# Kernel optimization log

Hardware: AMD Instinct MI355X
Metric: run time of the kernel (lower is better)

## Reference

```python
import jax, jax.numpy as jnp
import numpy as np

B, T, D = 4, 2048, 512
H, P = 8, 16
DH = D // H
C = 512
HF = WF = 64
RADIUS = 0.08


def setup_inputs() -> dict:
    key = jax.random.key(0)
    ks = jax.random.split(key, 8)
    s = 0.02
    return {
        "q": jax.random.normal(ks[0], (B, T, D), jnp.float32),
        "fmap": jax.random.normal(ks[1], (B, C, HF, WF), jnp.float32),
        "ref_xy": jax.random.uniform(ks[2], (B, T, 2), jnp.float32),
        # params ((in,out) layout; equals torch Linear with W.T)
        "Wv": jax.random.normal(ks[3], (C, D), jnp.float32) * s,      # 1x1 conv, no bias
        "W_off": jax.random.normal(ks[4], (D, H * P * 2), jnp.float32) * s,
        "b_off": jnp.zeros((H * P * 2,), jnp.float32),
        "W_w": jax.random.normal(ks[5], (D, H * P), jnp.float32) * s,
        "b_w": jnp.zeros((H * P,), jnp.float32),
        "W_out": jax.random.normal(ks[6], (D, D), jnp.float32) * s,
        "b_out": jnp.zeros((D,), jnp.float32),
    }


def _deform_attn(q, fmap, ref_xy, Wv, W_off, b_off, W_w, b_w, W_out, b_out):
    Bq, Tq, Dm = q.shape
    _, Cc, Hf, Wf = fmap.shape
    dh = Dm // H
    # value projection (1x1 conv) then split heads: (B,H,dh,Hf,Wf)
    v = jnp.einsum("bchw,cd->bdhw", fmap, Wv).reshape(Bq, H, dh, Hf, Wf)
    # flatten spatial for gather: (B,H,Hf*Wf,dh)
    vflat = v.transpose(0, 1, 3, 4, 2).reshape(Bq, H, Hf * Wf, dh)

    off = (q @ W_off + b_off).reshape(Bq, Tq, H, P, 2)
    attn = jax.nn.softmax((q @ W_w + b_w).reshape(Bq, Tq, H, P), axis=-1)

    samp = ref_xy[:, :, None, None, :] + RADIUS * off   # (B,T,H,P,2) in ~[0,1]
    g = samp * 2.0 - 1.0                                 # grid coords in [-1,1]
    # align_corners=True mapping to pixel coords
    ix = (g[..., 0] + 1.0) * 0.5 * (Wf - 1)              # (B,T,H,P)
    iy = (g[..., 1] + 1.0) * 0.5 * (Hf - 1)
    ix0 = jnp.floor(ix)
    iy0 = jnp.floor(iy)
    fx = ix - ix0
    fy = iy - iy0
    ix0i = ix0.astype(jnp.int32)
    iy0i = iy0.astype(jnp.int32)

    def corner(xi, yi, wgt):
        # wgt: bilinear weight * attention weight, (B,T,H,P)
        valid = (xi >= 0) & (xi < Wf) & (yi >= 0) & (yi < Hf)  # zeros padding
        xi_c = jnp.clip(xi, 0, Wf - 1)
        yi_c = jnp.clip(yi, 0, Hf - 1)
        idx = (yi_c * Wf + xi_c).transpose(0, 2, 1, 3).reshape(Bq, H, Tq * P)
        gat = jnp.take_along_axis(vflat, idx[..., None], axis=2)  # (B,H,T*P,dh)
        wm = (wgt * valid).transpose(0, 2, 1, 3).reshape(Bq, H, Tq * P)
        return gat * wm[..., None]

    # fold softmax weights into bilinear corner weights, then sum over points
    feat = (
        corner(ix0i,     iy0i,     (1 - fx) * (1 - fy) * attn)
        + corner(ix0i + 1, iy0i,     fx * (1 - fy) * attn)
        + corner(ix0i,     iy0i + 1, (1 - fx) * fy * attn)
        + corner(ix0i + 1, iy0i + 1, fx * fy * attn)
    )  # (B,H,T*P,dh)
    ctx = feat.reshape(Bq, H, Tq, P, dh).sum(axis=3)     # (B,H,T,dh)
    ctx = ctx.transpose(0, 2, 1, 3).reshape(Bq, Tq, Dm)  # concat heads
    return ctx @ W_out + b_out


def reference(q, fmap, ref_xy, Wv, W_off, b_off, W_w, b_w, W_out, b_out):
    return _deform_attn(q, fmap, ref_xy, Wv, W_off, b_off, W_w, b_w, W_out, b_out)
```

## Files before the change

kernel.cpp:

```cpp
#include <hip/hip_runtime.h>
#include <hip/hip_bf16.h>
#include <math.h>

constexpr int Bsz = 4, T = 2048, Hh = 8;
constexpr int HFi = 64, WFi = 64;
constexpr float RADIUS = 0.08f;

typedef __bf16 bf16x8 __attribute__((ext_vector_type(8)));
typedef float f32x4 __attribute__((ext_vector_type(4)));
typedef unsigned short u16x8 __attribute__((ext_vector_type(8)));

typedef const __attribute__((address_space(1))) void* gcptr;
typedef __attribute__((address_space(3))) void* lptr;

#define GLOAD_LDS16(g, l) \
  __builtin_amdgcn_global_load_lds((gcptr)(const void*)(g), (lptr)(void*)(l), 16, 0, 0)

union BU { __hip_bfloat16 b; unsigned short u; };

__global__ __launch_bounds__(256) void prep_kernel(
    const float* __restrict__ q, __hip_bfloat16* __restrict__ qsplit,
    const float* __restrict__ W_off, const float* __restrict__ W_w,
    const float* __restrict__ b_off, const float* __restrict__ b_w,
    __hip_bfloat16* __restrict__ Wcat, float* __restrict__ bias_cat,
    const float* __restrict__ Wv, __hip_bfloat16* __restrict__ WvT,
    const float* __restrict__ W_out, __hip_bfloat16* __restrict__ WoutT,
    const float* __restrict__ fmap, __hip_bfloat16* __restrict__ fmapT) {
  __shared__ float tile[64][65];
  const int blk = blockIdx.x;
  const int tid = threadIdx.x;
  if (blk < 4096) {
    const int idx = blk * 256 + tid;
    const int m = idx >> 7, kq = (idx & 127) * 4;
    float4 v = *(const float4*)&q[(size_t)m * 512 + kq];
    union { __hip_bfloat16 b[4]; ushort4 u; } hi, lo;
    float f[4] = {v.x, v.y, v.z, v.w};
#pragma unroll
    for (int i = 0; i < 4; ++i) {
      hi.b[i] = __float2bfloat16(f[i]);
      lo.b[i] = __float2bfloat16(f[i] - __bfloat162float(hi.b[i]));
    }
    *(ushort4*)&qsplit[(size_t)m * 1024 + kq] = hi.u;
    *(ushort4*)&qsplit[(size_t)m * 1024 + 512 + kq] = lo.u;
    return;
  }
  if (blk < 6400) {
    const int idx = (blk - 4096) * 256 + tid;
    const int n = idx / 1536, kp = idx % 1536;
    const int k = kp & 511;
    const float w = (n < 256) ? W_off[(size_t)k * 256 + n]
                              : W_w[(size_t)k * 128 + (n - 256)];
    const __hip_bfloat16 h = __float2bfloat16(w);
    const __hip_bfloat16 o =
        (kp < 1024) ? h : __float2bfloat16(w - __bfloat162float(h));
    Wcat[(size_t)n * 1536 + kp] = o;
    if (idx < 384) bias_cat[idx] = (idx < 256) ? b_off[idx] : b_w[idx - 256];
    return;
  }
  const float* src;
  __hip_bfloat16* dst;
  int ldin, ldout, r0, c0;
  if (blk < 6528) {
    const int t2 = blk - 6400;
    src = (t2 < 64) ? Wv : W_out;
    dst = (t2 < 64) ? WvT : WoutT;
    ldin = 512; ldout = 512;
    const int tl = t2 & 63;
    r0 = (tl >> 3) * 64; c0 = (tl & 7) * 64;
  } else {
    const int t3 = blk - 6528;
    const int b = t3 >> 9;
    const int tl = t3 & 511;
    r0 = (tl >> 6) * 64;
    c0 = (tl & 63) * 64;
    src = fmap + (size_t)b * 512 * 4096;
    dst = fmapT + (size_t)b * 4096 * 512;
    ldin = 4096; ldout = 512;
  }
  {
    const int tr = tid >> 2;
    const int tc = (tid & 3) * 16;
    const float* s = &src[(size_t)(r0 + tr) * ldin + c0 + tc];
#pragma unroll
    for (int j4 = 0; j4 < 4; ++j4) {
      float4 v = *(const float4*)&s[j4 * 4];
      tile[tr][tc + j4 * 4 + 0] = v.x;
      tile[tr][tc + j4 * 4 + 1] = v.y;
      tile[tr][tc + j4 * 4 + 2] = v.z;
      tile[tr][tc + j4 * 4 + 3] = v.w;
    }
    __syncthreads();
    const int oc = tid >> 2;
    const int rb = (tid & 3) * 16;
    u16x8 o0, o1;
#pragma unroll
    for (int j = 0; j < 8; ++j) {
      BU a, bz;
      a.b = __float2bfloat16(tile[rb + j][oc]);
      bz.b = __float2bfloat16(tile[rb + 8 + j][oc]);
      o0[j] = a.u;
      o1[j] = bz.u;
    }
    __hip_bfloat16* d = &dst[(size_t)(c0 + oc) * ldout + r0 + rb];
    *(u16x8*)d = o0;
    *(u16x8*)(d + 8) = o1;
  }
}

__global__ __launch_bounds__(256) void fused_gemm(
    const __hip_bfloat16* __restrict__ qsplit,
    const __hip_bfloat16* __restrict__ Wcat,
    const float* __restrict__ bias_cat, float* __restrict__ projbuf,
    const __hip_bfloat16* __restrict__ fmapT,
    const __hip_bfloat16* __restrict__ WvT, __hip_bfloat16* __restrict__ vflat) {
  __shared__ unsigned short As[128 * 64];
  __shared__ unsigned short Bs[128 * 64];
  const int blk = blockIdx.x;
  const int tid = threadIdx.x;
  const int lane = tid & 63;
  const int wave = tid >> 6;
  const int wm = (wave & 1) * 64, wn = (wave >> 1) * 64;
  const int l15 = lane & 15, quad = lane >> 4;

  const __hip_bfloat16 *A, *Bm;
  __hip_bfloat16* vout = nullptr;
  int lda, ldb, Kt, m0, n0, mode;
  bool awrap;
  if (blk < 512) {
    const int b = blk >> 7, r = blk & 127;
    m0 = (r >> 2) * 128;
    n0 = (r & 3) * 128;
    A = fmapT + (size_t)b * 4096 * 512; lda = 512;
    Bm = WvT; ldb = 512; Kt = 512;
    mode = 1; awrap = false;
    vout = vflat + (size_t)b * 8 * 4096 * 64;
  } else {
    const int pid = blk - 512;
    m0 = (pid & 63) * 128;
    n0 = (pid >> 6) * 128;
    A = qsplit; lda = 1024;
    Bm = Wcat; ldb = 1536; Kt = 1536;
    mode = 0; awrap = true;
  }

  f32x4 acc[4][4] = {};
  const int srow = lane >> 3;
  const int scol = (lane & 7) * 8;

  for (int k0 = 0; k0 < Kt; k0 += 64) {
    const int ka = (awrap && k0 >= 1024) ? k0 - 1024 : k0;
#pragma unroll
    for (int i = 0; i < 4; ++i) {
      const int j = wave * 4 + i;
      const int r = j * 8 + srow;
      GLOAD_LDS16(A + (size_t)(m0 + r) * lda + ka + scol, As + j * 512);
      GLOAD_LDS16(Bm + (size_t)(n0 + r) * ldb + k0 + scol, Bs + j * 512);
    }
    __syncthreads();
#pragma unroll
    for (int ks = 0; ks < 2; ++ks) {
      bf16x8 af[4], bfr[4];
#pragma unroll
      for (int i = 0; i < 4; ++i)
        af[i] = *(const bf16x8*)&As[(wm + i * 16 + l15) * 64 + ks * 32 + quad * 8];
#pragma unroll
      for (int j = 0; j < 4; ++j)
        bfr[j] = *(const bf16x8*)&Bs[(wn + j * 16 + l15) * 64 + ks * 32 + quad * 8];
#pragma unroll
      for (int i = 0; i < 4; ++i)
#pragma unroll
        for (int j = 0; j < 4; ++j)
          acc[i][j] = __builtin_amdgcn_mfma_f32_16x16x32_bf16(af[i], bfr[j], acc[i][j], 0, 0, 0);
    }
    __syncthreads();
  }

  if (mode == 0) {
#pragma unroll
    for (int i = 0; i < 4; ++i) {
      const int mbase = m0 + wm + i * 16 + quad * 4;
#pragma unroll
      for (int j = 0; j < 4; ++j) {
        const int n = n0 + wn + j * 16 + l15;
        const float bb = bias_cat[n];
#pragma unroll
        for (int r = 0; r < 4; ++r)
          projbuf[(size_t)(mbase + r) * 384 + n] = acc[i][j][r] + bb;
      }
    }
  } else {
#pragma unroll
    for (int i = 0; i < 4; ++i) {
      const int mbase = m0 + wm + i * 16 + quad * 4;
#pragma unroll
      for (int j = 0; j < 4; ++j) {
        const int ng = n0 + wn + j * 16 + l15;
        const int head = ng >> 6, dh = ng & 63;
#pragma unroll
        for (int r = 0; r < 4; ++r)
          vout[(size_t)head * (4096 * 64) + (size_t)(mbase + r) * 64 + dh] =
              __float2bfloat16(acc[i][j][r]);
      }
    }
  }
}

__global__ __launch_bounds__(256) void sample_kernel(
    const float* __restrict__ ref_xy, const float* __restrict__ projbuf,
    const unsigned int* __restrict__ vflat2, unsigned int* __restrict__ ctx2) {
  __shared__ float4 wsm[8][16];
  __shared__ int bsm[8][16];
  const int blk = blockIdx.x;
  const int bt = (blk & 7) * 1024 + (blk >> 3);
  const int b = bt >> 11;
  const int tid = threadIdx.x;
  const int wave = tid >> 6;
  const int lane = tid & 63;
  const int l31 = lane & 31;
  const bool hiHalf = lane >= 32;

  if (tid < 64) {
    const int h = tid >> 3, pi = tid & 7;
    const float ref_x = ref_xy[bt * 2 + 0];
    const float ref_y = ref_xy[bt * 2 + 1];
    const float* prow = projbuf + (size_t)bt * 384;
    const float* lg = prow + 256 + h * 16;
    float lv[16];
    float mx = -1e30f;
#pragma unroll
    for (int p = 0; p < 16; ++p) {
      lv[p] = lg[p];
      mx = fmaxf(mx, lv[p]);
    }
    float sum = 0.f;
#pragma unroll
    for (int p = 0; p < 16; ++p) {
      lv[p] = __expf(lv[p] - mx);
      sum += lv[p];
    }
    const float inv = 1.0f / sum;
    const float* of = prow + h * 32;
#pragma unroll
    for (int pq = 0; pq < 2; ++pq) {
      const int p = pi + pq * 8;
      const float aw = inv * lv[p];
      const float2 o2 = *(const float2*)&of[p * 2];
      const float ix = (ref_x + RADIUS * o2.x) * (float)(WFi - 1);
      const float iy = (ref_y + RADIUS * o2.y) * (float)(HFi - 1);
      const float ix0f = floorf(ix), iy0f = floorf(iy);
      const float fx = ix - ix0f, fy = iy - iy0f;
      const int ix0 = (int)ix0f, iy0 = (int)iy0f;

      float wx0 = 1.f - fx, wx1 = fx;
      float wy0 = 1.f - fy, wy1 = fy;
      if (ix0 == -1) { wx0 = fx; wx1 = 0.f; }
      if (ix0 == 63) { wx0 = 0.f; wx1 = 1.f - fx; }
      if (ix0 < -1 || ix0 > 63) { wx0 = 0.f; wx1 = 0.f; }
      if (iy0 == -1) { wy0 = fy; wy1 = 0.f; }
      if (iy0 == 63) { wy0 = 0.f; wy1 = 1.f - fy; }
      if (iy0 < -1 || iy0 > 63) { wy0 = 0.f; wy1 = 0.f; }
      const int xA = min(max(ix0, 0), WFi - 2);
      const int yA = min(max(iy0, 0), HFi - 2);

      wsm[h][p] = make_float4(wx0, wx1, wy0 * aw, wy1 * aw);
      bsm[h][p] = (yA * WFi + xA) * 32;
    }
  }
  __syncthreads();

  for (int h = wave; h < Hh; h += 4) {
    const float4* wq = &wsm[h][hiHalf ? 8 : 0];
    const int* bq = &bsm[h][hiHalf ? 8 : 0];
    const unsigned int* vb = vflat2 + (size_t)(b * 8 + h) * (4096 * 32) + l31;

    float acc0 = 0.f, acc1 = 0.f;
#pragma unroll
    for (int pp = 0; pp < 8; ++pp) {
      const float4 w4 = wq[pp];
      const unsigned int* r0 = vb + bq[pp];

      const unsigned int v00 = r0[0], v10 = r0[32];
      const unsigned int v01 = r0[2048], v11 = r0[2080];

      const float w00 = w4.x * w4.z, w10 = w4.y * w4.z;
      const float w01 = w4.x * w4.w, w11 = w4.y * w4.w;

      const float e00 = __uint_as_float(v00 << 16), o00 = __uint_as_float(v00 & 0xffff0000u);
      const float e10 = __uint_as_float(v10 << 16), o10 = __uint_as_float(v10 & 0xffff0000u);
      const float e01 = __uint_as_float(v01 << 16), o01 = __uint_as_float(v01 & 0xffff0000u);
      const float e11 = __uint_as_float(v11 << 16), o11 = __uint_as_float(v11 & 0xffff0000u);

      acc0 = fmaf(w00, e00, acc0);
      acc1 = fmaf(w00, o00, acc1);
      acc0 = fmaf(w10, e10, acc0);
      acc1 = fmaf(w10, o10, acc1);
      acc0 = fmaf(w01, e01, acc0);
      acc1 = fmaf(w01, o01, acc1);
      acc0 = fmaf(w11, e11, acc0);
      acc1 = fmaf(w11, o11, acc1);
    }

    acc0 += __shfl_xor(acc0, 32, 64);
    acc1 += __shfl_xor(acc1, 32, 64);
    if (!hiHalf) {
      union { __hip_bfloat16 b; unsigned short u; } c0, c1;
      c0.b = __float2bfloat16(acc0);
      c1.b = __float2bfloat16(acc1);
      ctx2[(size_t)bt * 256 + h * 32 + l31] = ((unsigned int)c1.u << 16) | c0.u;
    }
  }
}

__global__ __launch_bounds__(256) void outproj_kernel(
    const __hip_bfloat16* __restrict__ A, const __hip_bfloat16* __restrict__ Bm,
    const float* __restrict__ bias, float* __restrict__ C) {
  __shared__ unsigned short As[128 * 64];
  __shared__ unsigned short Bs[128 * 64];
  const int tid = threadIdx.x;
  const int lane = tid & 63;
  const int wave = tid >> 6;
  const int wm = (wave & 1) * 64, wn = (wave >> 1) * 64;
  const int l15 = lane & 15, quad = lane >> 4;
  const int m0 = blockIdx.x * 128, n0 = blockIdx.y * 128;

  f32x4 acc[4][4] = {};
  const int srow = lane >> 3;
  const int scol = (lane & 7) * 8;

  for (int k0 = 0; k0 < 512; k0 += 64) {
#pragma unroll
    for (int i = 0; i < 4; ++i) {
      const int j = wave * 4 + i;
      const int r = j * 8 + srow;
      GLOAD_LDS16(A + (size_t)(m0 + r) * 512 + k0 + scol, As + j * 512);
      GLOAD_LDS16(Bm + (size_t)(n0 + r) * 512 + k0 + scol, Bs + j * 512);
    }
    __syncthreads();
#pragma unroll
    for (int ks = 0; ks < 2; ++ks) {
      bf16x8 af[4], bfr[4];
#pragma unroll
      for (int i = 0; i < 4; ++i)
        af[i] = *(const bf16x8*)&As[(wm + i * 16 + l15) * 64 + ks * 32 + quad * 8];
#pragma unroll
      for (int j = 0; j < 4; ++j)
        bfr[j] = *(const bf16x8*)&Bs[(wn + j * 16 + l15) * 64 + ks * 32 + quad * 8];
#pragma unroll
      for (int i = 0; i < 4; ++i)
#pragma unroll
        for (int j = 0; j < 4; ++j)
          acc[i][j] = __builtin_amdgcn_mfma_f32_16x16x32_bf16(af[i], bfr[j], acc[i][j], 0, 0, 0);
    }
    __syncthreads();
  }

#pragma unroll
  for (int i = 0; i < 4; ++i) {
    const int mbase = m0 + wm + i * 16 + quad * 4;
#pragma unroll
    for (int j = 0; j < 4; ++j) {
      const int n = n0 + wn + j * 16 + l15;
      const float bb = bias[n];
#pragma unroll
      for (int r = 0; r < 4; ++r)
        C[(size_t)(mbase + r) * 512 + n] = acc[i][j][r] + bb;
    }
  }
}

extern "C" void kernel_launch(void* const* d_in, const int* in_sizes, int n_in,
                              void* d_out, int out_size, void* d_ws, size_t ws_size,
                              hipStream_t stream) {
  const float* q      = (const float*)d_in[0];
  const float* fmap   = (const float*)d_in[1];
  const float* ref_xy = (const float*)d_in[2];
  const float* Wv     = (const float*)d_in[3];
  const float* W_off  = (const float*)d_in[4];
  const float* b_off  = (const float*)d_in[5];
  const float* W_w    = (const float*)d_in[6];
  const float* b_w    = (const float*)d_in[7];
  const float* W_out  = (const float*)d_in[8];
  const float* b_out  = (const float*)d_in[9];
  float* out = (float*)d_out;

  char* ws = (char*)d_ws;
  __hip_bfloat16* qsplit = (__hip_bfloat16*)ws; ws += (size_t)8192 * 1024 * 2;
  __hip_bfloat16* Wcat   = (__hip_bfloat16*)ws; ws += (size_t)384 * 1536 * 2;
  float* bias_cat        = (float*)ws;          ws += 384 * 4;
  float* projbuf         = (float*)ws;          ws += (size_t)8192 * 384 * 4;
  __hip_bfloat16* fmapT  = (__hip_bfloat16*)ws; ws += (size_t)4 * 4096 * 512 * 2;
  __hip_bfloat16* WvT    = (__hip_bfloat16*)ws; ws += (size_t)512 * 512 * 2;
  __hip_bfloat16* WoutT  = (__hip_bfloat16*)ws; ws += (size_t)512 * 512 * 2;
  __hip_bfloat16* vflat  = (__hip_bfloat16*)ws; ws += (size_t)4 * 8 * 4096 * 64 * 2;
  __hip_bfloat16* ctxb   = (__hip_bfloat16*)ws; ws += (size_t)8192 * 512 * 2;

  prep_kernel<<<dim3(8576), 256, 0, stream>>>(
      q, qsplit, W_off, W_w, b_off, b_w, Wcat, bias_cat, Wv, WvT, W_out, WoutT,
      fmap, fmapT);

  fused_gemm<<<dim3(704), 256, 0, stream>>>(
      qsplit, Wcat, bias_cat, projbuf, fmapT, WvT, vflat);

  sample_kernel<<<dim3(Bsz * T), 256, 0, stream>>>(
      ref_xy, projbuf, (const unsigned int*)vflat, (unsigned int*)ctxb);

  outproj_kernel<<<dim3(64, 4), 256, 0, stream>>>(ctxb, WoutT, b_out, out);
}
```

Measured before the change: 200.4 us.

## Swizzle LDS tiles, split proj GEMM into narrower tiles, stage vflat stores via LDS

Applies an XOR swizzle to the LDS layout of A/B tiles in both GEMM kernels to reduce bank conflicts on the MFMA fragment reads. The projection GEMM uses 128x64 tiles and is scheduled first, which raises its block count from 192 to 384 and shortens the long-K tail. The value-projection epilogue now transposes through LDS so it can write 16-byte coalesced vectors instead of scattered 2-byte stores. The trade-off is more blocks that each reload A, plus an extra LDS round trip and barrier in the epilogue.

```diff
diff --git a/kernel.cpp b/kernel.cpp
--- a/kernel.cpp
+++ b/kernel.cpp
@@ -113,74 +113,60 @@
     const float* __restrict__ bias_cat, float* __restrict__ projbuf,
     const __hip_bfloat16* __restrict__ fmapT,
     const __hip_bfloat16* __restrict__ WvT, __hip_bfloat16* __restrict__ vflat) {
-  __shared__ unsigned short As[128 * 64];
-  __shared__ unsigned short Bs[128 * 64];
+  __shared__ unsigned short lds[2 * 128 * 64];
+  unsigned short* As = lds;
+  unsigned short* Bs = lds + 128 * 64;
   const int blk = blockIdx.x;
   const int tid = threadIdx.x;
   const int lane = tid & 63;
   const int wave = tid >> 6;
-  const int wm = (wave & 1) * 64, wn = (wave >> 1) * 64;
   const int l15 = lane & 15, quad = lane >> 4;
-
-  const __hip_bfloat16 *A, *Bm;
-  __hip_bfloat16* vout = nullptr;
-  int lda, ldb, Kt, m0, n0, mode;
-  bool awrap;
-  if (blk < 512) {
-    const int b = blk >> 7, r = blk & 127;
-    m0 = (r >> 2) * 128;
-    n0 = (r & 3) * 128;
-    A = fmapT + (size_t)b * 4096 * 512; lda = 512;
-    Bm = WvT; ldb = 512; Kt = 512;
-    mode = 1; awrap = false;
-    vout = vflat + (size_t)b * 8 * 4096 * 64;
-  } else {
-    const int pid = blk - 512;
-    m0 = (pid & 63) * 128;
-    n0 = (pid >> 6) * 128;
-    A = qsplit; lda = 1024;
-    Bm = Wcat; ldb = 1536; Kt = 1536;
-    mode = 0; awrap = true;
-  }
-
-  f32x4 acc[4][4] = {};
   const int srow = lane >> 3;
-  const int scol = (lane & 7) * 8;
-
-  for (int k0 = 0; k0 < Kt; k0 += 64) {
-    const int ka = (awrap && k0 >= 1024) ? k0 - 1024 : k0;
-#pragma unroll
-    for (int i = 0; i < 4; ++i) {
-      const int j = wave * 4 + i;
-      const int r = j * 8 + srow;
-      GLOAD_LDS16(A + (size_t)(m0 + r) * lda + ka + scol, As + j * 512);
-      GLOAD_LDS16(Bm + (size_t)(n0 + r) * ldb + k0 + scol, Bs + j * 512);
-    }
-    __syncthreads();
-#pragma unroll
-    for (int ks = 0; ks < 2; ++ks) {
-      bf16x8 af[4], bfr[4];
-#pragma unroll
-      for (int i = 0; i < 4; ++i)
-        af[i] = *(const bf16x8*)&As[(wm + i * 16 + l15) * 64 + ks * 32 + quad * 8];
-#pragma unroll
-      for (int j = 0; j < 4; ++j)
-        bfr[j] = *(const bf16x8*)&Bs[(wn + j * 16 + l15) * 64 + ks * 32 + quad * 8];
-#pragma unroll
-      for (int i = 0; i < 4; ++i)
-#pragma unroll
-        for (int j = 0; j < 4; ++j)
-          acc[i][j] = __builtin_amdgcn_mfma_f32_16x16x32_bf16(af[i], bfr[j], acc[i][j], 0, 0, 0);
-    }
-    __syncthreads();
-  }
-
-  if (mode == 0) {
+  const int scol = ((lane & 7) * 8) ^ ((srow & 1) * 32);
+  const int fxor = (l15 & 1) * 32;
+
+  if (blk < 384) {
+    const int m0 = (blk & 63) * 128;
+    const int n0 = (blk >> 6) * 64;
+    const int wm = (wave & 1) * 64, wn = (wave >> 1) * 32;
+    f32x4 acc[4][2] = {};
+    for (int k0 = 0; k0 < 1536; k0 += 64) {
+      const int ka = (k0 >= 1024) ? k0 - 1024 : k0;
+#pragma unroll
+      for (int i = 0; i < 4; ++i) {
+        const int j = wave * 4 + i;
+        const int r = j * 8 + srow;
+        GLOAD_LDS16(qsplit + (size_t)(m0 + r) * 1024 + ka + scol, As + j * 512);
+      }
+#pragma unroll
+      for (int i = 0; i < 2; ++i) {
+        const int j = wave * 2 + i;
+        const int r = j * 8 + srow;
+        GLOAD_LDS16(Wcat + (size_t)(n0 + r) * 1536 + k0 + scol, Bs + j * 512);
+      }
+      __syncthreads();
+#pragma unroll
+      for (int ks = 0; ks < 2; ++ks) {
+        bf16x8 af[4], bfr[2];
+#pragma unroll
+        for (int i = 0; i < 4; ++i)
+          af[i] = *(const bf16x8*)&As[(wm + i * 16 + l15) * 64 + ((ks * 32 + quad * 8) ^ fxor)];
+#pragma unroll
+        for (int j = 0; j < 2; ++j)
+          bfr[j] = *(const bf16x8*)&Bs[(wn + j * 16 + l15) * 64 + ((ks * 32 + quad * 8) ^ fxor)];
+#pragma unroll
+        for (int i = 0; i < 4; ++i)
+#pragma unroll
+          for (int j = 0; j < 2; ++j)
+            acc[i][j] = __builtin_amdgcn_mfma_f32_16x16x32_bf16(af[i], bfr[j], acc[i][j], 0, 0, 0);
+      }
+      __syncthreads();
+    }
 #pragma unroll
     for (int i = 0; i < 4; ++i) {
       const int mbase = m0 + wm + i * 16 + quad * 4;
 #pragma unroll
-      for (int j = 0; j < 4; ++j) {
+      for (int j = 0; j < 2; ++j) {
         const int n = n0 + wn + j * 16 + l15;
         const float bb = bias_cat[n];
 #pragma unroll
@@ -189,18 +175,64 @@
       }
     }
   } else {
+    const int vb = blk - 384;
+    const int b = vb >> 7, rr = vb & 127;
+    const int m0 = (rr >> 2) * 128;
+    const int n0 = (rr & 3) * 128;
+    const __hip_bfloat16* A = fmapT + (size_t)b * 4096 * 512;
+    __hip_bfloat16* vout = vflat + (size_t)b * 8 * 4096 * 64;
+    const int wm = (wave & 1) * 64, wn = (wave >> 1) * 64;
+    f32x4 acc[4][4] = {};
+    for (int k0 = 0; k0 < 512; k0 += 64) {
+#pragma unroll
+      for (int i = 0; i < 4; ++i) {
+        const int j = wave * 4 + i;
+        const int r = j * 8 + srow;
+        GLOAD_LDS16(A + (size_t)(m0 + r) * 512 + k0 + scol, As + j * 512);
+        GLOAD_LDS16(WvT + (size_t)(n0 + r) * 512 + k0 + scol, Bs + j * 512);
+      }
+      __syncthreads();
+#pragma unroll
+      for (int ks = 0; ks < 2; ++ks) {
+        bf16x8 af[4], bfr[4];
+#pragma unroll
+        for (int i = 0; i < 4; ++i)
+          af[i] = *(const bf16x8*)&As[(wm + i * 16 + l15) * 64 + ((ks * 32 + quad * 8) ^ fxor)];
+#pragma unroll
+        for (int j = 0; j < 4; ++j)
+          bfr[j] = *(const bf16x8*)&Bs[(wn + j * 16 + l15) * 64 + ((ks * 32 + quad * 8) ^ fxor)];
+#pragma unroll
+        for (int i = 0; i < 4; ++i)
+#pragma unroll
+          for (int j = 0; j < 4; ++j)
+            acc[i][j] = __builtin_amdgcn_mfma_f32_16x16x32_bf16(af[i], bfr[j], acc[i][j], 0, 0, 0);
+      }
+      __syncthreads();
+    }
+    unsigned short* Ct = lds;
 #pragma unroll
     for (int i = 0; i < 4; ++i) {
-      const int mbase = m0 + wm + i * 16 + quad * 4;
 #pragma unroll
       for (int j = 0; j < 4; ++j) {
-        const int ng = n0 + wn + j * 16 + l15;
-        const int head = ng >> 6, dh = ng & 63;
-#pragma unroll
-        for (int r = 0; r < 4; ++r)
-          vout[(size_t)head * (4096 * 64) + (size_t)(mbase + r) * 64 + dh] =
-              __float2bfloat16(acc[i][j][r]);
-      }
+        const int ngl = wn + j * 16 + l15;
+#pragma unroll
+        for (int r = 0; r < 4; ++r) {
+          const int sl = wm + i * 16 + quad * 4 + r;
+          BU u;
+          u.b = __float2bfloat16(acc[i][j][r]);
+          Ct[sl * 128 + ngl] = u.u;
+        }
+      }
+    }
+    __syncthreads();
+#pragma unroll
+    for (int c = 0; c < 8; ++c) {
+      const int sl = (tid >> 4) + c * 16;
+      const int chunk = tid & 15;
+      const int head = (n0 >> 6) + (chunk >> 3);
+      const int dh = (chunk & 7) * 8;
+      *(u16x8*)(vout + (size_t)head * (4096 * 64) + (size_t)(m0 + sl) * 64 + dh) =
+          *(const u16x8*)&Ct[sl * 128 + chunk * 8];
     }
   }
 }
@@ -322,10 +354,11 @@
   const int wm = (wave & 1) * 64, wn = (wave >> 1) * 64;
   const int l15 = lane & 15, quad = lane >> 4;
   const int m0 = blockIdx.x * 128, n0 = blockIdx.y * 128;
+  const int srow = lane >> 3;
+  const int scol = ((lane & 7) * 8) ^ ((srow & 1) * 32);
+  const int fxor = (l15 & 1) * 32;
 
   f32x4 acc[4][4] = {};
-  const int srow = lane >> 3;
-  const int scol = (lane & 7) * 8;
 
   for (int k0 = 0; k0 < 512; k0 += 64) {
 #pragma unroll
@@ -341,10 +374,10 @@
       bf16x8 af[4], bfr[4];
 #pragma unroll
       for (int i = 0; i < 4; ++i)
-        af[i] = *(const bf16x8*)&As[(wm + i * 16 + l15) * 64 + ks * 32 + quad * 8];
+        af[i] = *(const bf16x8*)&As[(wm + i * 16 + l15) * 64 + ((ks * 32 + quad * 8) ^ fxor)];
 #pragma unroll
       for (int j = 0; j < 4; ++j)
-        bfr[j] = *(const bf16x8*)&Bs[(wn + j * 16 + l15) * 64 + ks * 32 + quad * 8];
+        bfr[j] = *(const bf16x8*)&Bs[(wn + j * 16 + l15) * 64 + ((ks * 32 + quad * 8) ^ fxor)];
 #pragma unroll
       for (int i = 0; i < 4; ++i)
 #pragma unroll
@@ -398,7 +431,7 @@
       q, qsplit, W_off, W_w, b_off, b_w, Wcat, bias_cat, Wv, WvT, W_out, WoutT,
       fmap, fmapT);
 
-  fused_gemm<<<dim3(704), 256, 0, stream>>>(
+  fused_gemm<<<dim3(896), 256, 0, stream>>>(
       qsplit, Wcat, bias_cat, projbuf, fmapT, WvT, vflat);
 
   sample_kernel<<<dim3(Bsz * T), 256, 0, stream>>>(
```

Result: faster. 195.1 us (-2.6%).
